# Kernel tuning notes

Measured on AMD Instinct MI355X. Metric: run time of the kernel, lower is better.

The kernel has to match this reference:

```python
import jax, jax.numpy as jnp
import numpy as np

N = 50000        # nodes
E = 800000       # edges (before self loops)
IN = 128         # in_channels
HID = 32         # hidden_channels (per head)
HEADS = 4
OUT = 10         # out_channels (classes)
G = 64           # graphs in batch
NEG_SLOPE = 0.2  # PyG GATConv default leaky relu slope


def setup_inputs() -> dict:
    key = jax.random.key(0)
    ks = jax.random.split(key, 12)
    s = 0.05
    return {
        "x": jax.random.normal(ks[0], (N, IN), jnp.float32),
        "W1": jax.random.normal(ks[1], (IN, HEADS * HID), jnp.float32) * s,
        "a1_src": jax.random.normal(ks[2], (HEADS, HID), jnp.float32) * s,
        "a1_dst": jax.random.normal(ks[3], (HEADS, HID), jnp.float32) * s,
        "b1": jnp.zeros((HEADS * HID,), jnp.float32),
        "W2": jax.random.normal(ks[4], (HEADS * HID, HEADS * HID), jnp.float32) * s,
        "a2_src": jax.random.normal(ks[5], (HEADS, HID), jnp.float32) * s,
        "a2_dst": jax.random.normal(ks[6], (HEADS, HID), jnp.float32) * s,
        "b2": jnp.zeros((HEADS * HID,), jnp.float32),
        "Wl": jax.random.normal(ks[7], (HEADS * HID, OUT), jnp.float32) * s,
        "bl": jnp.zeros((OUT,), jnp.float32),
        "edge_index": jax.random.randint(ks[8], (2, E), 0, N, jnp.int32),
        "batch": jnp.sort(jax.random.randint(ks[9], (N,), 0, G, jnp.int32)),
    }


def gat_conv(x, src, dst, W, a_src, a_dst, b):
    """PyG GATConv (concat=True, self loops already in src/dst). Eval mode: no dropout."""
    n = x.shape[0]
    h = (x @ W).reshape(n, HEADS, HID)                       # [N,H,C]
    al_s = jnp.einsum('nhc,hc->nh', h, a_src)                # [N,H]
    al_d = jnp.einsum('nhc,hc->nh', h, a_dst)
    e = jax.nn.leaky_relu(al_s[src] + al_d[dst], NEG_SLOPE)  # [Etot,H]
    # segment softmax over destination node neighborhoods
    m = jax.ops.segment_max(e, dst, num_segments=n)
    m = jnp.where(jnp.isfinite(m), m, 0.0)
    p = jnp.exp(e - m[dst])
    z = jax.ops.segment_sum(p, dst, num_segments=n)
    alpha = p / (z[dst] + 1e-16)                             # [Etot,H]
    out = jax.ops.segment_sum(h[src] * alpha[:, :, None], dst, num_segments=n)
    return out.reshape(n, HEADS * HID) + b


def reference(x, W1, a1_src, a1_dst, b1, W2, a2_src, a2_dst, b2, Wl, bl,
              edge_index, batch):
    n = x.shape[0]
    loops = jnp.arange(n, dtype=edge_index.dtype)
    src = jnp.concatenate([edge_index[0], loops])
    dst = jnp.concatenate([edge_index[1], loops])

    h = jax.nn.elu(gat_conv(x, src, dst, W1, a1_src, a1_dst, b1))
    h = gat_conv(h, src, dst, W2, a2_src, a2_dst, b2)

    # global_mean_pool over graph ids
    counts = jax.ops.segment_sum(jnp.ones((n,), h.dtype), batch, num_segments=G)
    pooled = jax.ops.segment_sum(h, batch, num_segments=G) / jnp.maximum(counts, 1.0)[:, None]

    logits = pooled @ Wl + bl
    return jax.nn.softmax(logits, axis=1)
```

## Files before the change

### kernel.cpp

```cpp
#include <hip/hip_runtime.h>
#include <hip/hip_bf16.h>
#include <math.h>

#define HEADS 4
#define HID 32
#define FDIM 128
#define OUTC 10
#define NEG 0.2f
#define ECAP 512
#define BCAP 5440

typedef __attribute__((ext_vector_type(4))) float f32x4;
typedef __attribute__((ext_vector_type(2))) float f32x2;
typedef __attribute__((ext_vector_type(8))) short bf16x8;

static __device__ __forceinline__ float lrelu(float v) { return v > 0.f ? v : NEG * v; }

static __device__ __forceinline__ unsigned bfr(float f) {
  unsigned u = __float_as_uint(f);
  return (u + 0x7fffu + ((u >> 16) & 1u)) >> 16;
}
static __device__ __forceinline__ float blo(unsigned u) { return __uint_as_float(u << 16); }
static __device__ __forceinline__ float bhi(unsigned u) { return __uint_as_float(u & 0xffff0000u); }

#define CHUNK 4096

__global__ __launch_bounds__(256) void k_bin(
    const int* __restrict__ ei, int* __restrict__ gbcur,
    int2* __restrict__ bbuf, int E, int n) {
  __shared__ int h[256];
  __shared__ int cur[256];
  int tid = threadIdx.x;
  h[tid] = 0;
  __syncthreads();
  int base = blockIdx.x * CHUNK;
  int tot = E + n;
  #pragma unroll
  for (int r = 0; r < 16; ++r) {
    int e = base + r * 256 + tid;
    if (e < tot) {
      int dst = (e < E) ? ei[E + e] : (e - E);
      atomicAdd(&h[dst >> 8], 1);
    }
  }
  __syncthreads();
  if (h[tid]) cur[tid] = tid * BCAP + atomicAdd(&gbcur[tid], h[tid]);
  __syncthreads();
  #pragma unroll
  for (int r = 0; r < 16; ++r) {
    int e = base + r * 256 + tid;
    if (e < tot) {
      int src = (e < E) ? ei[e] : (e - E);
      int dst = (e < E) ? ei[E + e] : (e - E);
      int pos = atomicAdd(&cur[dst >> 8], 1);
      bbuf[pos] = make_int2(src, dst);
    }
  }
}

__global__ __launch_bounds__(256) void k_build(
    const int2* __restrict__ bbuf, const int* __restrict__ gbcur,
    int* __restrict__ offs, int* __restrict__ csr, int* __restrict__ dpos,
    int n) {
  __shared__ int deg[256];
  __shared__ int sc[256];
  __shared__ int cur[256];
  int b = blockIdx.x;
  int tid = threadIdx.x;
  int ebeg = b * BCAP;
  int eend = ebeg + gbcur[b];
  deg[tid] = 0;
  __syncthreads();
  for (int i = ebeg + tid; i < eend; i += 256)
    atomicAdd(&deg[bbuf[i].y & 255], 1);
  __syncthreads();
  int v = deg[tid];
  sc[tid] = v;
  __syncthreads();
  #pragma unroll
  for (int off = 1; off < 256; off <<= 1) {
    int t = (tid >= off) ? sc[tid - off] : 0;
    __syncthreads();
    sc[tid] += t;
    __syncthreads();
  }
  int excl = sc[tid] - v;
  int dst0 = b * 256 + tid;
  if (dst0 < n) offs[dst0] = ebeg + excl;
  cur[tid] = ebeg + excl;
  __syncthreads();
  for (int i = ebeg + tid; i < eend; i += 256) {
    int2 sd = bbuf[i];
    int pos = atomicAdd(&cur[sd.y & 255], 1);
    csr[pos] = sd.x;
    dpos[pos] = sd.y;
  }
}

__global__ __launch_bounds__(256) void k_prep(
    const float* __restrict__ W1, const float* __restrict__ W2,
    const float* __restrict__ a1s, const float* __restrict__ a1d,
    const float* __restrict__ a2s, const float* __restrict__ a2d,
    uint4* __restrict__ WF) {
  int layer = blockIdx.y;
  const float* W = layer ? W2 : W1;
  __shared__ float wa[128][8];
  int tid = threadIdx.x;
  #pragma unroll
  for (int q = 0; q < 4; ++q) {
    int e = tid * 4 + q;
    int k = e >> 3, c = e & 7;
    int h = c & 3;
    const float* av = (c < 4 ? (layer ? a2s : a1s) : (layer ? a2d : a1d)) + h * 32;
    const float* wr = W + (size_t)k * 128 + h * 32;
    float s = 0.f;
    #pragma unroll
    for (int j = 0; j < 32; j += 4) {
      float4 wv = *reinterpret_cast<const float4*>(wr + j);
      float4 a4 = *reinterpret_cast<const float4*>(av + j);
      s += wv.x * a4.x + wv.y * a4.y + wv.z * a4.z + wv.w * a4.w;
    }
    wa[k][c] = s;
  }
  __syncthreads();
  int gid = blockIdx.x * 256 + tid;
  if (gid >= 2304) return;
  int lane = gid & 63, frag = gid >> 6;
  int t = frag / 9, ct = frag - t * 9;
  int quad = lane >> 4, r = lane & 15;
  int kbase = t * 32 + quad * 8;
  unsigned v[8];
  if (ct < 8) {
    int col = ct * 16 + r;
    #pragma unroll
    for (int j = 0; j < 8; ++j) v[j] = bfr(W[(size_t)(kbase + j) * 128 + col]);
  } else if (r < 8) {
    #pragma unroll
    for (int j = 0; j < 8; ++j) v[j] = bfr(wa[kbase + j][r]);
  } else {
    #pragma unroll
    for (int j = 0; j < 8; ++j) v[j] = 0;
  }
  uint4 pk;
  pk.x = v[0] | (v[1] << 16);
  pk.y = v[2] | (v[3] << 16);
  pk.z = v[4] | (v[5] << 16);
  pk.w = v[6] | (v[7] << 16);
  WF[layer * 2304 + gid] = pk;
}

template<bool BF16IN>
__global__ __launch_bounds__(256) void k_mm(
    const void* __restrict__ Xv, const uint4* __restrict__ WF,
    unsigned char* __restrict__ H, float* __restrict__ AL, int n) {
  __shared__ uint4 wf[2304];
  int tid = threadIdx.x;
  #pragma unroll
  for (int i = 0; i < 9; ++i) wf[i * 256 + tid] = WF[i * 256 + tid];
  __syncthreads();
  int lane = tid & 63, wid = tid >> 6;
  int quad = lane >> 4, r = lane & 15;
  int rowbase = blockIdx.x * 64 + wid * 16;
  int arow = rowbase + r;
  int arowc = arow < n ? arow : 0;
  const bf16x8* wfs = (const bf16x8*)wf;

  f32x4 acc[9];
  #pragma unroll
  for (int ct = 0; ct < 9; ++ct) acc[ct] = 0;

  #pragma unroll
  for (int t = 0; t < 4; ++t) {
    bf16x8 a;
    if (BF16IN) {
      const uint4* xp = reinterpret_cast<const uint4*>(Xv) + (size_t)arowc * 16;
      uint4 u = xp[t * 4 + quad];
      a = *reinterpret_cast<const bf16x8*>(&u);
    } else {
      const float* xp = reinterpret_cast<const float*>(Xv) + (size_t)arowc * 128 + quad * 8;
      float4 x0 = *reinterpret_cast<const float4*>(xp + t * 32);
      float4 x1 = *reinterpret_cast<const float4*>(xp + t * 32 + 4);
      a[0] = (short)bfr(x0.x); a[1] = (short)bfr(x0.y);
      a[2] = (short)bfr(x0.z); a[3] = (short)bfr(x0.w);
      a[4] = (short)bfr(x1.x); a[5] = (short)bfr(x1.y);
      a[6] = (short)bfr(x1.z); a[7] = (short)bfr(x1.w);
    }
    #pragma unroll
    for (int ct = 0; ct < 9; ++ct)
      acc[ct] = __builtin_amdgcn_mfma_f32_16x16x32_bf16(
          a, wfs[(t * 9 + ct) * 64 + lane], acc[ct], 0, 0, 0);
  }

  int orow0 = rowbase + quad * 4;
  #pragma unroll
  for (int rr = 0; rr < 4; ++rr) {
    int orow = orow0 + rr;
    if (orow < n) {
      unsigned char* hp = H + (size_t)orow * 128 + r;
      #pragma unroll
      for (int ct = 0; ct < 8; ++ct) {
        unsigned p8 = __builtin_amdgcn_cvt_pk_fp8_f32(acc[ct][rr], acc[ct][rr], 0, false);
        hp[ct * 16] = (unsigned char)(p8 & 0xffu);
      }
      if (r < 8) AL[(size_t)orow * 8 + r] = acc[8][rr];
    }
  }
}

template<bool ELU_OUT, bool POOL>
__global__ __launch_bounds__(256) void k_agg(
    const unsigned char* __restrict__ H, const float* __restrict__ AL,
    const int* __restrict__ offs, const int* __restrict__ csr,
    const int* __restrict__ dpos, const int* __restrict__ gbcur,
    const float* __restrict__ bias, unsigned short* __restrict__ OUT,
    const int* __restrict__ batch, float* __restrict__ pooled,
    int* __restrict__ gcnt, int n) {
  __shared__ __align__(16) char smem[ECAP * 4 + ECAP * 16];
  int* s_l = (int*)smem;
  float (*p_l)[4] = (float(*)[4])(smem + ECAP * 4);
  float (*o_l)[132] = (float(*)[132])smem;
  __shared__ int g_l[16];
  int tid = threadIdx.x;
  int lane = tid & 63;
  int r = lane & 15;
  int gg = (tid >> 6) * 4 + (lane >> 4);
  int nbase = blockIdx.x * 16;
  int node = nbase + gg;
  bool nvalid = node < n;
  int nodec = nvalid ? node : 0;
  int bkt = nbase >> 8;
  int bend = bkt * BCAP + gbcur[bkt];
  int beg = offs[nodec];
  int nxt = nodec + 1;
  int end = nvalid ? ((nxt >= n || (nxt & 255) == 0) ? bend : offs[nxt]) : beg;
  int ebeg = offs[nbase];
  int nend = nbase + 16;
  int eend = (nend >= n || (nend & 255) == 0) ? bend : offs[nend];
  int hsel = r >> 2;
  const uint2* hb = reinterpret_cast<const uint2*>(H) + r;

  if (POOL && r == 0) g_l[gg] = nvalid ? batch[node] : -1;

  float z = 0.f;
  float acc[8];
  #pragma unroll
  for (int k = 0; k < 8; ++k) acc[k] = 0.f;

  for (int c0 = ebeg; c0 < eend; c0 += ECAP) {
    int clen = min(ECAP, eend - c0);
    __syncthreads();
    for (int i = tid; i < clen; i += 256) {
      int s = csr[c0 + i];
      int d = dpos[c0 + i];
      float4 as_ = *reinterpret_cast<const float4*>(AL + (size_t)s * 8);
      float4 ad = *reinterpret_cast<const float4*>(AL + (size_t)d * 8 + 4);
      s_l[i] = s;
      float4 p;
      p.x = __expf(lrelu(as_.x + ad.x));
      p.y = __expf(lrelu(as_.y + ad.y));
      p.z = __expf(lrelu(as_.z + ad.z));
      p.w = __expf(lrelu(as_.w + ad.w));
      *reinterpret_cast<float4*>(&p_l[i][0]) = p;
    }
    __syncthreads();
    int lo = max(beg, c0), hi = min(end, c0 + clen);
    int cnt = hi - lo;
    int lbase = lo - c0;
    for (int j0 = 0; j0 < cnt; j0 += 4) {
      int j1 = j0 + 1, j2 = j0 + 2, j3 = j0 + 3;
      bool v1 = j1 < cnt, v2 = j2 < cnt, v3 = j3 < cnt;
      int jB = lbase + (v1 ? j1 : j0);
      int jC = lbase + (v2 ? j2 : j0);
      int jD = lbase + (v3 ? j3 : j0);
      int jA = lbase + j0;
      int sA = s_l[jA], sB = s_l[jB], sC = s_l[jC], sD = s_l[jD];
      float pA = p_l[jA][hsel];
      float pB = v1 ? p_l[jB][hsel] : 0.f;
      float pC = v2 ? p_l[jC][hsel] : 0.f;
      float pD = v3 ? p_l[jD][hsel] : 0.f;
      z += (pA + pB) + (pC + pD);
      uint2 uA = hb[(size_t)sA * 16];
      uint2 uB = hb[(size_t)sB * 16];
      uint2 uC = hb[(size_t)sC * 16];
      uint2 uD = hb[(size_t)sD * 16];
      {
        f32x2 h0 = __builtin_amdgcn_cvt_pk_f32_fp8(uA.x, false);
        f32x2 h1 = __builtin_amdgcn_cvt_pk_f32_fp8(uA.x, true);
        f32x2 h2 = __builtin_amdgcn_cvt_pk_f32_fp8(uA.y, false);
        f32x2 h3 = __builtin_amdgcn_cvt_pk_f32_fp8(uA.y, true);
        acc[0] = fmaf(pA, h0.x, acc[0]); acc[1] = fmaf(pA, h0.y, acc[1]);
        acc[2] = fmaf(pA, h1.x, acc[2]); acc[3] = fmaf(pA, h1.y, acc[3]);
        acc[4] = fmaf(pA, h2.x, acc[4]); acc[5] = fmaf(pA, h2.y, acc[5]);
        acc[6] = fmaf(pA, h3.x, acc[6]); acc[7] = fmaf(pA, h3.y, acc[7]);
      }
      {
        f32x2 h0 = __builtin_amdgcn_cvt_pk_f32_fp8(uB.x, false);
        f32x2 h1 = __builtin_amdgcn_cvt_pk_f32_fp8(uB.x, true);
        f32x2 h2 = __builtin_amdgcn_cvt_pk_f32_fp8(uB.y, false);
        f32x2 h3 = __builtin_amdgcn_cvt_pk_f32_fp8(uB.y, true);
        acc[0] = fmaf(pB, h0.x, acc[0]); acc[1] = fmaf(pB, h0.y, acc[1]);
        acc[2] = fmaf(pB, h1.x, acc[2]); acc[3] = fmaf(pB, h1.y, acc[3]);
        acc[4] = fmaf(pB, h2.x, acc[4]); acc[5] = fmaf(pB, h2.y, acc[5]);
        acc[6] = fmaf(pB, h3.x, acc[6]); acc[7] = fmaf(pB, h3.y, acc[7]);
      }
      {
        f32x2 h0 = __builtin_amdgcn_cvt_pk_f32_fp8(uC.x, false);
        f32x2 h1 = __builtin_amdgcn_cvt_pk_f32_fp8(uC.x, true);
        f32x2 h2 = __builtin_amdgcn_cvt_pk_f32_fp8(uC.y, false);
        f32x2 h3 = __builtin_amdgcn_cvt_pk_f32_fp8(uC.y, true);
        acc[0] = fmaf(pC, h0.x, acc[0]); acc[1] = fmaf(pC, h0.y, acc[1]);
        acc[2] = fmaf(pC, h1.x, acc[2]); acc[3] = fmaf(pC, h1.y, acc[3]);
        acc[4] = fmaf(pC, h2.x, acc[4]); acc[5] = fmaf(pC, h2.y, acc[5]);
        acc[6] = fmaf(pC, h3.x, acc[6]); acc[7] = fmaf(pC, h3.y, acc[7]);
      }
      {
        f32x2 h0 = __builtin_amdgcn_cvt_pk_f32_fp8(uD.x, false);
        f32x2 h1 = __builtin_amdgcn_cvt_pk_f32_fp8(uD.x, true);
        f32x2 h2 = __builtin_amdgcn_cvt_pk_f32_fp8(uD.y, false);
        f32x2 h3 = __builtin_amdgcn_cvt_pk_f32_fp8(uD.y, true);
        acc[0] = fmaf(pD, h0.x, acc[0]); acc[1] = fmaf(pD, h0.y, acc[1]);
        acc[2] = fmaf(pD, h1.x, acc[2]); acc[3] = fmaf(pD, h1.y, acc[3]);
        acc[4] = fmaf(pD, h2.x, acc[4]); acc[5] = fmaf(pD, h2.y, acc[5]);
        acc[6] = fmaf(pD, h3.x, acc[6]); acc[7] = fmaf(pD, h3.y, acc[7]);
      }
    }
  }

  float inv = 1.f / (z + 1e-16f);
  int f0 = r * 8;
  float4 b0 = *reinterpret_cast<const float4*>(bias + f0);
  float4 b1 = *reinterpret_cast<const float4*>(bias + f0 + 4);
  float o[8];
  o[0] = acc[0] * inv + b0.x; o[1] = acc[1] * inv + b0.y;
  o[2] = acc[2] * inv + b0.z; o[3] = acc[3] * inv + b0.w;
  o[4] = acc[4] * inv + b1.x; o[5] = acc[5] * inv + b1.y;
  o[6] = acc[6] * inv + b1.z; o[7] = acc[7] * inv + b1.w;
  if (ELU_OUT) {
    #pragma unroll
    for (int k = 0; k < 8; ++k) o[k] = o[k] > 0.f ? o[k] : expm1f(o[k]);
  }

  if (!POOL) {
    if (nvalid) {
      uint4 pk;
      pk.x = bfr(o[0]) | (bfr(o[1]) << 16);
      pk.y = bfr(o[2]) | (bfr(o[3]) << 16);
      pk.z = bfr(o[4]) | (bfr(o[5]) << 16);
      pk.w = bfr(o[6]) | (bfr(o[7]) << 16);
      reinterpret_cast<uint4*>(OUT)[(size_t)node * 16 + r] = pk;
    }
  } else {
    __syncthreads();
    *reinterpret_cast<float4*>(&o_l[gg][f0]) = make_float4(o[0], o[1], o[2], o[3]);
    *reinterpret_cast<float4*>(&o_l[gg][f0 + 4]) = make_float4(o[4], o[5], o[6], o[7]);
    __syncthreads();
    if (tid < 128) {
      int f = tid;
      float accp = 0.f; int cur = -1;
      #pragma unroll
      for (int i = 0; i < 16; ++i) {
        int g = g_l[i];
        if (g != cur) {
          if (cur >= 0) atomicAdd(&pooled[(size_t)cur * 128 + f], accp);
          cur = g; accp = 0.f;
        }
        if (g >= 0) accp += o_l[i][f];
      }
      if (cur >= 0) atomicAdd(&pooled[(size_t)cur * 128 + f], accp);
    } else if (tid == 128) {
      int cur = -1, c = 0;
      #pragma unroll
      for (int i = 0; i < 16; ++i) {
        int g = g_l[i];
        if (g != cur) { if (cur >= 0) atomicAdd(&gcnt[cur], c); cur = g; c = 0; }
        if (g >= 0) ++c;
      }
      if (cur >= 0) atomicAdd(&gcnt[cur], c);
    }
  }
}

__global__ void k_head(const float* __restrict__ pooled, const int* __restrict__ gcnt,
                       const float* __restrict__ Wl, const float* __restrict__ bl,
                       float* __restrict__ out) {
  int g = blockIdx.x;
  int lane = threadIdx.x;
  float cnt = fmaxf((float)gcnt[g], 1.f);
  float pA = pooled[(size_t)g * 128 + lane] / cnt;
  float pB = pooled[(size_t)g * 128 + lane + 64] / cnt;
  float l[OUTC];
  #pragma unroll
  for (int o = 0; o < OUTC; ++o) {
    float s = pA * Wl[lane * OUTC + o] + pB * Wl[(lane + 64) * OUTC + o];
    #pragma unroll
    for (int off = 32; off; off >>= 1) s += __shfl_xor(s, off);
    l[o] = s + bl[o];
  }
  float mx = l[0];
  #pragma unroll
  for (int o = 1; o < OUTC; ++o) mx = fmaxf(mx, l[o]);
  float se = 0.f;
  #pragma unroll
  for (int o = 0; o < OUTC; ++o) { l[o] = __expf(l[o] - mx); se += l[o]; }
  if (lane == 0) {
    float inv = 1.f / se;
    #pragma unroll
    for (int o = 0; o < OUTC; ++o) out[g * OUTC + o] = l[o] * inv;
  }
}

extern "C" void kernel_launch(void* const* d_in, const int* in_sizes, int n_in,
                              void* d_out, int out_size, void* d_ws, size_t ws_size,
                              hipStream_t stream) {
  const float* x   = (const float*)d_in[0];
  const float* W1  = (const float*)d_in[1];
  const float* a1s = (const float*)d_in[2];
  const float* a1d = (const float*)d_in[3];
  const float* b1  = (const float*)d_in[4];
  const float* W2  = (const float*)d_in[5];
  const float* a2s = (const float*)d_in[6];
  const float* a2d = (const float*)d_in[7];
  const float* b2  = (const float*)d_in[8];
  const float* Wl  = (const float*)d_in[9];
  const float* bl  = (const float*)d_in[10];
  const int* ei    = (const int*)d_in[11];
  const int* batch = (const int*)d_in[12];
  const int N = in_sizes[12];
  const int E = in_sizes[11] / 2;
  const int G = out_size / OUTC;
  float* out = (float*)d_out;
  (void)n_in; (void)ws_size;

  const int tot = E + N;
  const int NB = (N + 255) / 256;

  char* w = (char*)d_ws;
  auto alloc = [&](size_t bytes) { char* p = w; w += (bytes + 255) & ~(size_t)255; return (void*)p; };
  unsigned char* H = (unsigned char*)alloc((size_t)N * FDIM);
  unsigned short* ACT = (unsigned short*)alloc((size_t)N * FDIM * sizeof(unsigned short));
  float* AL     = (float*)alloc((size_t)N * 8 * sizeof(float));
  uint4* WF     = (uint4*)alloc(2 * 2304 * sizeof(uint4));
  int*   offs   = (int*)alloc((size_t)N * sizeof(int));
  int*   csr    = (int*)alloc((size_t)NB * BCAP * sizeof(int));
  int*   dpos   = (int*)alloc((size_t)NB * BCAP * sizeof(int));
  int2*  bbuf   = (int2*)alloc((size_t)NB * BCAP * sizeof(int2));
  char* z0 = w;
  int*   gbcur  = (int*)alloc(256 * sizeof(int));
  int*   gcnt   = (int*)alloc((size_t)G * sizeof(int));
  float* pooled = (float*)alloc((size_t)G * FDIM * sizeof(float));
  size_t zbytes = (size_t)(w - z0);
  hipMemsetAsync(z0, 0, zbytes, stream);

  int ab4 = (tot + CHUNK - 1) / CHUNK;
  k_bin<<<ab4, 256, 0, stream>>>(ei, gbcur, bbuf, E, N);
  k_build<<<NB, 256, 0, stream>>>(bbuf, gbcur, offs, csr, dpos, N);

  k_prep<<<dim3(9, 2), 256, 0, stream>>>(W1, W2, a1s, a1d, a2s, a2d, WF);

  int gb = (N + 63) / 64;
  int ab = (N + 15) / 16;
  k_mm<false><<<gb, 256, 0, stream>>>(x, WF, H, AL, N);
  k_agg<true, false><<<ab, 256, 0, stream>>>(H, AL, offs, csr, dpos, gbcur, b1, ACT, batch, pooled, gcnt, N);
  k_mm<true><<<gb, 256, 0, stream>>>(ACT, WF + 2304, H, AL, N);
  k_agg<false, true><<<ab, 256, 0, stream>>>(H, AL, offs, csr, dpos, gbcur, b2, nullptr, batch, pooled, gcnt, N);

  k_head<<<G, 64, 0, stream>>>(pooled, gcnt, Wl, bl, out);
}
```

Measured before the change: 216.4 us.

## Replace two-pass bucket binning with global degree count, scan, and atomic scatter CSR build

The CSR build used to bin edges into per-256-node buckets through an intermediate int2 buffer, then sort each bucket in LDS. It now counts per-node in-degree with global atomics, scans per block to get offsets (placing the self-loop first), and scatters each edge directly with a global atomic cursor per destination node. This drops the bbuf round trip and one full pass over the edges, at the cost of one more launch, many contended global atomics, and a nondeterministic edge order within each row.

```diff
diff --git a/kernel.cpp b/kernel.cpp
--- a/kernel.cpp
+++ b/kernel.cpp
@@ -20,61 +20,24 @@
   unsigned u = __float_as_uint(f);
   return (u + 0x7fffu + ((u >> 16) & 1u)) >> 16;
 }
-static __device__ __forceinline__ float blo(unsigned u) { return __uint_as_float(u << 16); }
-static __device__ __forceinline__ float bhi(unsigned u) { return __uint_as_float(u & 0xffff0000u); }
-
-#define CHUNK 4096
-
-__global__ __launch_bounds__(256) void k_bin(
-    const int* __restrict__ ei, int* __restrict__ gbcur,
-    int2* __restrict__ bbuf, int E, int n) {
-  __shared__ int h[256];
-  __shared__ int cur[256];
-  int tid = threadIdx.x;
-  h[tid] = 0;
-  __syncthreads();
-  int base = blockIdx.x * CHUNK;
-  int tot = E + n;
-  #pragma unroll
-  for (int r = 0; r < 16; ++r) {
-    int e = base + r * 256 + tid;
-    if (e < tot) {
-      int dst = (e < E) ? ei[E + e] : (e - E);
-      atomicAdd(&h[dst >> 8], 1);
-    }
-  }
-  __syncthreads();
-  if (h[tid]) cur[tid] = tid * BCAP + atomicAdd(&gbcur[tid], h[tid]);
-  __syncthreads();
-  #pragma unroll
-  for (int r = 0; r < 16; ++r) {
-    int e = base + r * 256 + tid;
-    if (e < tot) {
-      int src = (e < E) ? ei[e] : (e - E);
-      int dst = (e < E) ? ei[E + e] : (e - E);
-      int pos = atomicAdd(&cur[dst >> 8], 1);
-      bbuf[pos] = make_int2(src, dst);
-    }
-  }
-}
-
-__global__ __launch_bounds__(256) void k_build(
-    const int2* __restrict__ bbuf, const int* __restrict__ gbcur,
-    int* __restrict__ offs, int* __restrict__ csr, int* __restrict__ dpos,
+
+
+__global__ __launch_bounds__(256) void k_count(
+    const int* __restrict__ ei, int* __restrict__ deg, int E) {
+  int i = blockIdx.x * 256 + threadIdx.x;
+  int stride = gridDim.x * 256;
+  for (int e = i; e < E; e += stride)
+    atomicAdd(&deg[ei[E + e]], 1);
+}
+
+__global__ __launch_bounds__(256) void k_scan(
+    const int* __restrict__ deg, int* __restrict__ offs, int* __restrict__ cur,
+    int* __restrict__ csr, int* __restrict__ dpos, int* __restrict__ gbcur,
     int n) {
-  __shared__ int deg[256];
   __shared__ int sc[256];
-  __shared__ int cur[256];
-  int b = blockIdx.x;
-  int tid = threadIdx.x;
-  int ebeg = b * BCAP;
-  int eend = ebeg + gbcur[b];
-  deg[tid] = 0;
-  __syncthreads();
-  for (int i = ebeg + tid; i < eend; i += 256)
-    atomicAdd(&deg[bbuf[i].y & 255], 1);
-  __syncthreads();
-  int v = deg[tid];
+  int b = blockIdx.x, tid = threadIdx.x;
+  int dst0 = b * 256 + tid;
+  int v = (dst0 < n) ? deg[dst0] + 1 : 0;
   sc[tid] = v;
   __syncthreads();
   #pragma unroll
@@ -85,15 +48,26 @@
     __syncthreads();
   }
   int excl = sc[tid] - v;
-  int dst0 = b * 256 + tid;
-  if (dst0 < n) offs[dst0] = ebeg + excl;
-  cur[tid] = ebeg + excl;
-  __syncthreads();
-  for (int i = ebeg + tid; i < eend; i += 256) {
-    int2 sd = bbuf[i];
-    int pos = atomicAdd(&cur[sd.y & 255], 1);
-    csr[pos] = sd.x;
-    dpos[pos] = sd.y;
+  if (dst0 < n) {
+    int base = b * BCAP + excl;
+    offs[dst0] = base;
+    csr[base] = dst0;
+    dpos[base] = dst0;
+    cur[dst0] = base + 1;
+  }
+  if (tid == 255) gbcur[b] = sc[255];
+}
+
+__global__ __launch_bounds__(256) void k_scatter(
+    const int* __restrict__ ei, int* __restrict__ cur,
+    int* __restrict__ csr, int* __restrict__ dpos, int E) {
+  int i = blockIdx.x * 256 + threadIdx.x;
+  int stride = gridDim.x * 256;
+  for (int e = i; e < E; e += stride) {
+    int s = ei[e], d = ei[E + e];
+    int pos = atomicAdd(&cur[d], 1);
+    csr[pos] = s;
+    dpos[pos] = d;
   }
 }
 
@@ -431,7 +405,6 @@
   float* out = (float*)d_out;
   (void)n_in; (void)ws_size;
 
-  const int tot = E + N;
   const int NB = (N + 255) / 256;
 
   char* w = (char*)d_ws;
@@ -441,19 +414,20 @@
   float* AL     = (float*)alloc((size_t)N * 8 * sizeof(float));
   uint4* WF     = (uint4*)alloc(2 * 2304 * sizeof(uint4));
   int*   offs   = (int*)alloc((size_t)N * sizeof(int));
+  int*   cur    = (int*)alloc((size_t)N * sizeof(int));
   int*   csr    = (int*)alloc((size_t)NB * BCAP * sizeof(int));
   int*   dpos   = (int*)alloc((size_t)NB * BCAP * sizeof(int));
-  int2*  bbuf   = (int2*)alloc((size_t)NB * BCAP * sizeof(int2));
   char* z0 = w;
+  int*   deg    = (int*)alloc((size_t)N * sizeof(int));
   int*   gbcur  = (int*)alloc(256 * sizeof(int));
   int*   gcnt   = (int*)alloc((size_t)G * sizeof(int));
   float* pooled = (float*)alloc((size_t)G * FDIM * sizeof(float));
   size_t zbytes = (size_t)(w - z0);
   hipMemsetAsync(z0, 0, zbytes, stream);
 
-  int ab4 = (tot + CHUNK - 1) / CHUNK;
-  k_bin<<<ab4, 256, 0, stream>>>(ei, gbcur, bbuf, E, N);
-  k_build<<<NB, 256, 0, stream>>>(bbuf, gbcur, offs, csr, dpos, N);
+  k_count<<<1024, 256, 0, stream>>>(ei, deg, E);
+  k_scan<<<NB, 256, 0, stream>>>(deg, offs, cur, csr, dpos, gbcur, N);
+  k_scatter<<<1024, 256, 0, stream>>>(ei, cur, csr, dpos, E);
 
   k_prep<<<dim3(9, 2), 256, 0, stream>>>(W1, W2, a1s, a1d, a2s, a2d, WF);
 
```

New measurement: 279.4 us. +29.1%, slower.
